# Optimization experiments

Hardware: AMD Instinct MI355X
Metric: run time of the kernel (lower is better)

Reference implementation:

```python
import jax, jax.numpy as jnp
import numpy as np

LARGE = 1e10  # sentinel used to mask non-edge entries before top-2 min


def setup_inputs() -> dict:
    B, m, n = 128, 512, 1024
    row_weight = 8  # check-node degree of the LDPC code
    key = jax.random.key(0)
    k1, k2 = jax.random.split(key)
    soft_input = jax.random.normal(k1, (B, n), dtype=jnp.float32)
    labels = jax.random.randint(k2, (B, n), 0, 2).astype(jnp.int64)
    # structured sparse parity-check matrix: each check touches `row_weight` variables
    rng = np.random.default_rng(0)
    cols = np.argsort(rng.random((m, n)), axis=1)[:, :row_weight]
    H_np = np.zeros((m, n), dtype=np.int32)
    H_np[np.arange(m)[:, None], cols] = 1
    H = jnp.asarray(H_np)
    normalizer = jnp.full((1,), -2.0, dtype=jnp.float32)  # decoder_check_normalizor init
    return {"soft_input": soft_input, "labels": labels, "H": H,
            "normalizer": normalizer, "num_iterations": 10}


def _bp_forward(soft_input, H, normalizer, num_iterations):
    Hf = H.astype(jnp.float32)              # [m, n]
    sup = (1.0 - Hf)[None]                  # supplement matrix, [1, m, n]
    norm = jax.nn.softplus(normalizer)      # [1], NMS scaling factor

    def step(soft, _):
        # variable -> check messages: [B, m, n]
        vc = soft[:, None, :] * Hf
        # sign part: product of message signs per check row (off-edge entries are +1)
        s = jnp.sign(sup + vc)
        row_prod = jnp.prod(s, axis=2, keepdims=True)       # [B, m, 1]
        result_sign = row_prod * Hf * s                     # extrinsic sign, [B, m, n]
        # magnitude part: min-sum with top-2 smallest magnitudes per check row
        avc = jnp.abs(vc)
        proc = jnp.where(avc * Hf == 0, LARGE, avc * Hf)
        neg_top2 = jax.lax.top_k(-proc, 2)[0]               # [B, m, 2]
        smallest = -neg_top2[..., 0:1]
        second = -neg_top2[..., 1:2]
        updated = jnp.where(avc == smallest, second, smallest) * Hf
        cv = norm * updated * jax.lax.stop_gradient(result_sign)
        new_soft = soft + jnp.sum(cv, axis=1)               # marginalize, [B, n]
        return new_soft, new_soft

    _, outs = jax.lax.scan(step, soft_input, None, length=num_iterations)
    return jnp.concatenate([soft_input[None], outs], axis=0)  # [iters+1, B, n]


def reference(soft_input, labels, H, normalizer, num_iterations):
    soft_output_stack = _bp_forward(soft_input, H, normalizer, num_iterations)
    return soft_output_stack, labels
```

## Files before the change

kernel.cpp:

```cpp
#include <hip/hip_runtime.h>

#define RW 8
#define LARGE_V 1e10f
#define MAXI 10
#define NV 1024
#define NC 512
#define SCALE 1048576.0f
#define INV_SCALE (1.0f / 1048576.0f)

__global__ __launch_bounds__(64) void extract_cols_kernel(const int* __restrict__ H,
                                                          int* __restrict__ cols) {
    const int i    = blockIdx.x;
    const int lane = threadIdx.x;

    const int4* rp = (const int4*)(H + (size_t)i * NV + lane * 16);
    int v[16];
    #pragma unroll
    for (int q = 0; q < 4; ++q) {
        int4 x = rp[q];
        v[q * 4 + 0] = x.x; v[q * 4 + 1] = x.y;
        v[q * 4 + 2] = x.z; v[q * 4 + 3] = x.w;
    }
    int cnt = 0;
    #pragma unroll
    for (int e = 0; e < 16; ++e) cnt += (v[e] != 0);
    int pre = cnt;
    #pragma unroll
    for (int d = 1; d < 64; d <<= 1) {
        int o = __shfl_up(pre, d);
        if (lane >= d) pre += o;
    }
    pre -= cnt;
    int k = 0;
    #pragma unroll
    for (int e = 0; e < 16; ++e) {
        if (v[e] != 0) {
            if (pre + k < RW) cols[i * RW + pre + k] = lane * 16 + e;
            ++k;
        }
    }
}

__global__ __launch_bounds__(1024) void bp_kernel(const float* __restrict__ soft_in,
                                                  const int* __restrict__ labels,
                                                  const int* __restrict__ cols,
                                                  const float* __restrict__ normalizer,
                                                  float* __restrict__ out,
                                                  int B, int niter) {
    __shared__ float stack[MAXI + 1][NV];
    __shared__ int   iacc[NV];

    const int b   = blockIdx.x;
    const int tid = threadIdx.x;

    {
        stack[0][tid] = soft_in[(size_t)b * NV + tid];
        iacc[tid] = 0;
        float* out_labels = out + (size_t)(niter + 1) * B * NV;
        out_labels[(size_t)b * NV + tid] = (float)labels[(size_t)b * NV + tid];
    }

    int c[4];
    {
        int4 a4 = *(const int4*)(cols + (tid >> 1) * RW + (tid & 1) * 4);
        c[0] = a4.x & (NV - 1); c[1] = a4.y & (NV - 1);
        c[2] = a4.z & (NV - 1); c[3] = a4.w & (NV - 1);
    }
    const float norm = log1pf(expf(normalizer[0]));
    __syncthreads();

    int ni = (niter > MAXI) ? MAXI : niter;

    for (int t = 0; t < ni; ++t) {
        const float* cur = stack[t];

        float a[4], p[4];
        unsigned int sb[4];
        unsigned int sxa = 0;
        bool anyz = false;
        #pragma unroll
        for (int k = 0; k < 4; ++k) {
            float vv = cur[c[k]];
            unsigned int bits = __float_as_uint(vv);
            sb[k] = bits & 0x80000000u;
            sxa ^= sb[k];
            float av = fabsf(vv);
            a[k] = av;
            anyz = anyz || (av == 0.0f);
            p[k] = (av == 0.0f) ? LARGE_V : av;
        }
        sxa = (sxa & 0x80000000u) | (anyz ? 1u : 0u);
        unsigned int oth = (unsigned int)__shfl_xor((int)sxa, 1);
        const unsigned int prodsign = (sxa ^ oth) & 0x80000000u;
        const bool zz = ((sxa | oth) & 1u) != 0u;

        float l0 = fminf(p[0], p[1]), h0 = fmaxf(p[0], p[1]);
        float l1 = fminf(p[2], p[3]), h1 = fmaxf(p[2], p[3]);
        float m1 = fminf(l0, l1);
        float m2 = fminf(fmaxf(l0, l1), fminf(h0, h1));
        float m1o = __shfl_xor(m1, 1);
        float m2o = __shfl_xor(m2, 1);
        const float mn1 = fminf(m1, m1o);
        const float mn2 = fminf(fmaxf(m1, m1o), fminf(m2, m2o));

        const float nm1 = norm * mn1, nm2 = norm * mn2;
        #pragma unroll
        for (int k = 0; k < 4; ++k) {
            float mag = (a[k] == mn1) ? nm2 : nm1;
            unsigned int mb = __float_as_uint(mag) ^ (prodsign ^ sb[k]);
            float msg = zz ? 0.0f : __uint_as_float(mb);
            atomicAdd(&iacc[c[k]], __float2int_rn(msg * SCALE));
        }
        __syncthreads();

        {
            float sp = stack[t][tid];
            int   ia = iacc[tid];
            stack[t + 1][tid] = sp + (float)ia * INV_SCALE;
            iacc[tid] = 0;
        }
        __syncthreads();
    }

    const int total4 = (ni + 1) * (NV / 4);
    for (int idx = tid; idx < total4; idx += 1024) {
        int slice = idx >> 8;
        int pos   = idx & 255;
        float4 val = *(const float4*)&stack[slice][pos * 4];
        *(float4*)(out + ((size_t)slice * B + b) * NV + (size_t)pos * 4) = val;
    }
}

extern "C" void kernel_launch(void* const* d_in, const int* in_sizes, int n_in,
                              void* d_out, int out_size, void* d_ws, size_t ws_size,
                              hipStream_t stream) {
    const float* soft_in    = (const float*)d_in[0];
    const int*   labels     = (const int*)d_in[1];
    const int*   H          = (const int*)d_in[2];
    const float* normalizer = (const float*)d_in[3];

    const int B     = in_sizes[0] / NV;
    const int niter = out_size / (B * NV) - 2;

    int* cols = (int*)d_ws;

    extract_cols_kernel<<<NC, 64, 0, stream>>>(H, cols);
    bp_kernel<<<B, 1024, 0, stream>>>(soft_in, labels, cols, normalizer,
                                      (float*)d_out, B, niter);
}
```

Baseline: 21.62 us.

## Stream per-iteration outputs directly and move label conversion into setup kernel

Removes the per-block shared-memory stack of all iterations and writes each iteration's soft output straight to global memory inside the loop, with a single soft buffer in LDS. The label int-to-float conversion moves from the BP kernel into the column-extraction kernel as extra blocks, and message construction is done in integer fixed-point with cheaper sign handling. Barriers use a raw s_waitcnt plus s_barrier, and the accumulator is read and reset with atomicExch. This cuts LDS footprint and the tail copy, but global stores are now interleaved with the iteration loop and the iteration cap is removed.

```diff
diff --git a/kernel.cpp b/kernel.cpp
--- a/kernel.cpp
+++ b/kernel.cpp
@@ -2,63 +2,77 @@
 
 #define RW 8
 #define LARGE_V 1e10f
-#define MAXI 10
 #define NV 1024
 #define NC 512
 #define SCALE 1048576.0f
 #define INV_SCALE (1.0f / 1048576.0f)
 
-__global__ __launch_bounds__(64) void extract_cols_kernel(const int* __restrict__ H,
-                                                          int* __restrict__ cols) {
-    const int i    = blockIdx.x;
+#define LDS_BARRIER() do { \
+    asm volatile("s_waitcnt lgkmcnt(0)" ::: "memory"); \
+    __builtin_amdgcn_s_barrier(); \
+} while (0)
+
+__global__ __launch_bounds__(64) void setup_kernel(const int* __restrict__ H,
+                                                   int* __restrict__ cols,
+                                                   const int* __restrict__ labels,
+                                                   float* __restrict__ out_labels,
+                                                   int lab_total) {
+    const int blk  = blockIdx.x;
     const int lane = threadIdx.x;
 
-    const int4* rp = (const int4*)(H + (size_t)i * NV + lane * 16);
-    int v[16];
-    #pragma unroll
-    for (int q = 0; q < 4; ++q) {
-        int4 x = rp[q];
-        v[q * 4 + 0] = x.x; v[q * 4 + 1] = x.y;
-        v[q * 4 + 2] = x.z; v[q * 4 + 3] = x.w;
-    }
-    int cnt = 0;
-    #pragma unroll
-    for (int e = 0; e < 16; ++e) cnt += (v[e] != 0);
-    int pre = cnt;
-    #pragma unroll
-    for (int d = 1; d < 64; d <<= 1) {
-        int o = __shfl_up(pre, d);
-        if (lane >= d) pre += o;
-    }
-    pre -= cnt;
-    int k = 0;
-    #pragma unroll
-    for (int e = 0; e < 16; ++e) {
-        if (v[e] != 0) {
-            if (pre + k < RW) cols[i * RW + pre + k] = lane * 16 + e;
-            ++k;
+    if (blk < NC) {
+        const int4* rp = (const int4*)(H + (size_t)blk * NV + lane * 16);
+        int v[16];
+        #pragma unroll
+        for (int q = 0; q < 4; ++q) {
+            int4 x = rp[q];
+            v[q * 4 + 0] = x.x; v[q * 4 + 1] = x.y;
+            v[q * 4 + 2] = x.z; v[q * 4 + 3] = x.w;
+        }
+        int cnt = 0;
+        #pragma unroll
+        for (int e = 0; e < 16; ++e) cnt += (v[e] != 0);
+        int pre = cnt;
+        #pragma unroll
+        for (int d = 1; d < 64; d <<= 1) {
+            int o = __shfl_up(pre, d);
+            if (lane >= d) pre += o;
+        }
+        pre -= cnt;
+        int k = 0;
+        #pragma unroll
+        for (int e = 0; e < 16; ++e) {
+            if (v[e] != 0) {
+                if (pre + k < RW) cols[blk * RW + pre + k] = lane * 16 + e;
+                ++k;
+            }
+        }
+    } else {
+        const int base = (blk - NC) * 1024 + lane * 16;
+        if (base + 15 < lab_total) {
+            #pragma unroll
+            for (int q = 0; q < 4; ++q) {
+                int4 x = *(const int4*)(labels + base + q * 4);
+                float4 f;
+                f.x = (float)x.x; f.y = (float)x.y;
+                f.z = (float)x.z; f.w = (float)x.w;
+                *(float4*)(out_labels + base + q * 4) = f;
+            }
         }
     }
 }
 
 __global__ __launch_bounds__(1024) void bp_kernel(const float* __restrict__ soft_in,
-                                                  const int* __restrict__ labels,
                                                   const int* __restrict__ cols,
                                                   const float* __restrict__ normalizer,
                                                   float* __restrict__ out,
                                                   int B, int niter) {
-    __shared__ float stack[MAXI + 1][NV];
+    __shared__ float soft[NV];
     __shared__ int   iacc[NV];
 
     const int b   = blockIdx.x;
     const int tid = threadIdx.x;
-
-    {
-        stack[0][tid] = soft_in[(size_t)b * NV + tid];
-        iacc[tid] = 0;
-        float* out_labels = out + (size_t)(niter + 1) * B * NV;
-        out_labels[(size_t)b * NV + tid] = (float)labels[(size_t)b * NV + tid];
-    }
+    const size_t BN = (size_t)B * NV;
 
     int c[4];
     {
@@ -67,20 +81,21 @@
         c[2] = a4.z & (NV - 1); c[3] = a4.w & (NV - 1);
     }
     const float norm = log1pf(expf(normalizer[0]));
-    __syncthreads();
 
-    int ni = (niter > MAXI) ? MAXI : niter;
+    float sv = soft_in[(size_t)b * NV + tid];
+    soft[tid] = sv;
+    iacc[tid] = 0;
+    out[(size_t)b * NV + tid] = sv;
+    LDS_BARRIER();
 
-    for (int t = 0; t < ni; ++t) {
-        const float* cur = stack[t];
-
+    for (int t = 0; t < niter; ++t) {
         float a[4], p[4];
         unsigned int sb[4];
         unsigned int sxa = 0;
         bool anyz = false;
         #pragma unroll
         for (int k = 0; k < 4; ++k) {
-            float vv = cur[c[k]];
+            float vv = soft[c[k]];
             unsigned int bits = __float_as_uint(vv);
             sb[k] = bits & 0x80000000u;
             sxa ^= sb[k];
@@ -103,31 +118,26 @@
         const float mn1 = fminf(m1, m1o);
         const float mn2 = fminf(fmaxf(m1, m1o), fminf(m2, m2o));
 
-        const float nm1 = norm * mn1, nm2 = norm * mn2;
+        int im1 = zz ? 0 : __float2int_rn(norm * mn1 * SCALE);
+        int im2 = zz ? 0 : __float2int_rn(norm * mn2 * SCALE);
+        int nm1i = -im1, nm2i = -im2;
         #pragma unroll
         for (int k = 0; k < 4; ++k) {
-            float mag = (a[k] == mn1) ? nm2 : nm1;
-            unsigned int mb = __float_as_uint(mag) ^ (prodsign ^ sb[k]);
-            float msg = zz ? 0.0f : __uint_as_float(mb);
-            atomicAdd(&iacc[c[k]], __float2int_rn(msg * SCALE));
+            bool sel = (a[k] == mn1);
+            bool neg = ((prodsign ^ sb[k]) != 0u);
+            int mag = sel ? im2 : im1;
+            int nmg = sel ? nm2i : nm1i;
+            atomicAdd(&iacc[c[k]], neg ? nmg : mag);
         }
-        __syncthreads();
+        LDS_BARRIER();
 
         {
-            float sp = stack[t][tid];
-            int   ia = iacc[tid];
-            stack[t + 1][tid] = sp + (float)ia * INV_SCALE;
-            iacc[tid] = 0;
+            int ia = atomicExch(&iacc[tid], 0);
+            sv += (float)ia * INV_SCALE;
+            soft[tid] = sv;
+            out[(size_t)(t + 1) * BN + (size_t)b * NV + tid] = sv;
         }
-        __syncthreads();
-    }
-
-    const int total4 = (ni + 1) * (NV / 4);
-    for (int idx = tid; idx < total4; idx += 1024) {
-        int slice = idx >> 8;
-        int pos   = idx & 255;
-        float4 val = *(const float4*)&stack[slice][pos * 4];
-        *(float4*)(out + ((size_t)slice * B + b) * NV + (size_t)pos * 4) = val;
+        LDS_BARRIER();
     }
 }
 
@@ -144,7 +154,12 @@
 
     int* cols = (int*)d_ws;
 
-    extract_cols_kernel<<<NC, 64, 0, stream>>>(H, cols);
-    bp_kernel<<<B, 1024, 0, stream>>>(soft_in, labels, cols, normalizer,
+    const int lab_total  = B * NV;
+    const int lab_blocks = (lab_total + 1023) / 1024;
+    float* out_labels = (float*)d_out + (size_t)(niter + 1) * lab_total;
+
+    setup_kernel<<<NC + lab_blocks, 64, 0, stream>>>(H, cols, labels,
+                                                     out_labels, lab_total);
+    bp_kernel<<<B, 1024, 0, stream>>>(soft_in, cols, normalizer,
                                       (float*)d_out, B, niter);
 }
```

New measurement: 20.55 us. 5.0% less time.
